# Optimization experiments

Measured on AMD Instinct MI355X. Metric: run time of the kernel, lower is better.

## Reference

```python
import jax, jax.numpy as jnp
import numpy as np

N_NODES = 50000
N_EDGES = 800000
F_IN = 128
HIDDEN = 128
F_OUT = 64
BN_EPS = 1e-5


def setup_inputs() -> dict:
    key = jax.random.key(0)
    ks = jax.random.split(key, 8)
    features = jax.random.normal(ks[0], (N_NODES, F_IN), dtype=jnp.float32)
    W1 = jax.random.normal(ks[1], (2 * F_IN, HIDDEN), dtype=jnp.float32) * 0.05
    b1 = jnp.zeros((HIDDEN,), dtype=jnp.float32)
    gamma = jnp.ones((HIDDEN,), dtype=jnp.float32)
    beta = jnp.zeros((HIDDEN,), dtype=jnp.float32)
    W2 = jax.random.normal(ks[2], (2 * HIDDEN, F_OUT), dtype=jnp.float32) * 0.05
    b2 = jnp.zeros((F_OUT,), dtype=jnp.float32)
    edge_vals = jax.random.uniform(ks[3], (N_EDGES,), dtype=jnp.float32)
    edge_src = jax.random.randint(ks[4], (N_EDGES,), 0, N_NODES, dtype=jnp.int32)
    edge_dst = jax.random.randint(ks[5], (N_EDGES,), 0, N_NODES, dtype=jnp.int32)
    return {"features": features, "W1": W1, "b1": b1, "gamma": gamma,
            "beta": beta, "W2": W2, "b2": b2, "edge_vals": edge_vals,
            "edge_src": edge_src, "edge_dst": edge_dst}


def _spmm(edge_vals, edge_src, edge_dst, x):
    # agg[i] = sum_{e: dst_e == i} w_e * x[src_e]   (sparse adjacency @ x)
    msgs = edge_vals[:, None] * x[edge_src]          # [E, d]
    return jax.ops.segment_sum(msgs, edge_dst, num_segments=N_NODES)


def _batchnorm(x, gamma, beta):
    # BatchNorm1d in training mode: batch stats, biased variance
    mean = jnp.mean(x, axis=0)
    var = jnp.mean(jnp.square(x - mean), axis=0)
    return gamma * (x - mean) * jax.lax.rsqrt(var + BN_EPS) + beta


def reference(features, W1, b1, gamma, beta, W2, b2, edge_vals, edge_src, edge_dst):
    # Layer 1: SpMM -> concat -> linear -> batchnorm -> relu  (dropout is a no-op, p=0)
    agg = _spmm(edge_vals, edge_src, edge_dst, features)     # [N, F_IN]
    s = jnp.concatenate([agg, features], axis=1)             # [N, 2*F_IN]
    h = s @ W1 + b1                                          # [N, HIDDEN]
    h = jax.nn.relu(_batchnorm(h, gamma, beta))
    # Layer 2: SpMM -> concat -> linear (identity act, no norm)
    agg2 = _spmm(edge_vals, edge_src, edge_dst, h)           # [N, HIDDEN]
    s2 = jnp.concatenate([agg2, h], axis=1)                  # [N, 2*HIDDEN]
    out = s2 @ W2 + b2                                       # [N, F_OUT]
    return out
```

## Files before the change

kernel.cpp:

```cpp
#include <hip/hip_runtime.h>

#define N_NODES 50000
#define N_EDGES 800000
#define F_IN    128
#define HID     128
#define F_OUT   64
#define BN_EPS  1e-5f

#define NRANGES 196
#define NCHUNKS 196
#define CHUNK   4096
#define CVT_BLOCKS 3125
#define PREPW_BLOCKS 24

typedef __bf16 bf16x8 __attribute__((ext_vector_type(8)));
typedef float  f32x4  __attribute__((ext_vector_type(4)));

static inline size_t align_up(size_t x, size_t a){ return (x + a - 1) / a * a; }

__device__ __forceinline__ float bflo(unsigned u){ return __uint_as_float(u << 16); }
__device__ __forceinline__ float bfhi(unsigned u){ return __uint_as_float(u & 0xffff0000u); }
__device__ __forceinline__ unsigned packbf(float a, float b){
  __bf16 ha = (__bf16)a, hb = (__bf16)b;
  unsigned short ua = __builtin_bit_cast(unsigned short, ha);
  unsigned short ub = __builtin_bit_cast(unsigned short, hb);
  return (unsigned)ua | ((unsigned)ub << 16);
}


__global__ __launch_bounds__(256) void k_setup(
    const int* __restrict__ dst, const float* __restrict__ X,
    const float* __restrict__ W1, const float* __restrict__ W2,
    int* __restrict__ Hcr, __bf16* __restrict__ Sx,
    __bf16* __restrict__ W1f, __bf16* __restrict__ W2f, float* __restrict__ bn_acc){
  __shared__ int hist[NRANGES];
  int b = blockIdx.x, t = threadIdx.x;
  if(b < NCHUNKS){
    if(t < NRANGES) hist[t] = 0;
    __syncthreads();
    int e0 = b * CHUNK;
    #pragma unroll
    for(int k = 0; k < CHUNK / 256; k++){
      int e = e0 + k * 256 + t;
      if(e < N_EDGES) atomicAdd(&hist[dst[e] >> 8], 1);
    }
    __syncthreads();
    if(t < NRANGES) Hcr[b * NRANGES + t] = hist[t];
  } else if(b < NCHUNKS + CVT_BLOCKS){
    int bb = b - NCHUNKS;
    if(bb == 0) bn_acc[t] = 0.f;
    int idx = bb * 256 + t;
    int n = idx >> 4;
    int c = (idx & 15) * 8;
    const float* xp = X + (size_t)n * F_IN + c;
    f32x4 x0 = *(const f32x4*)xp;
    f32x4 x1 = *(const f32x4*)(xp + 4);
    bf16x8 v;
    #pragma unroll
    for(int i = 0; i < 4; i++){ v[i] = (__bf16)x0[i]; v[4 + i] = (__bf16)x1[i]; }
    *(bf16x8*)(Sx + (size_t)n * 128 + c) = v;
  } else {
    int s = (b - NCHUNKS - CVT_BLOCKS) * 256 + t;
    if(s < 4096){
      int ks = s >> 9, rem = s & 511, nf = rem >> 6, l = rem & 63;
      int k = ks * 32 + (l >> 4) * 8, c = nf * 16 + (l & 15);
      bf16x8 v;
      #pragma unroll
      for(int i = 0; i < 8; i++) v[i] = (__bf16)W1[(size_t)(k + i) * HID + c];
      *(bf16x8*)(W1f + ((size_t)s << 3)) = v;
    } else {
      int q = s - 4096;
      int ks = q >> 9, rem = q & 511, nf = rem >> 6, l = rem & 63;
      int k = ks * 32 + (l >> 4) * 8, c = nf * 16 + (l & 15);
      bf16x8 v;
      #pragma unroll
      for(int i = 0; i < 8; i++){
        int kk = k + i;
        float val = (c < 64) ? W2[(size_t)kk * F_OUT + c]
                             : W2[(size_t)(HID + kk) * F_OUT + (c - 64)];
        v[i] = (__bf16)val;
      }
      *(bf16x8*)(W2f + ((size_t)q << 3)) = v;
    }
  }
}


__global__ __launch_bounds__(256) void k_scanR(int* __restrict__ Hcr, int* __restrict__ rtot){
  __shared__ int s[256];
  int r = blockIdx.x, t = threadIdx.x;
  int v = (t < NCHUNKS) ? Hcr[t * NRANGES + r] : 0;
  s[t] = v;
  __syncthreads();
  for(int off = 1; off < 256; off <<= 1){
    int u = (t >= off) ? s[t - off] : 0;
    __syncthreads();
    s[t] += u;
    __syncthreads();
  }
  if(t < NCHUNKS) Hcr[t * NRANGES + r] = s[t] - v;
  if(t == NCHUNKS - 1) rtot[r] = s[t];
}


__global__ __launch_bounds__(256) void k_pass2(const int* __restrict__ dst, const int* __restrict__ src,
    const float* __restrict__ vals, const int* __restrict__ Hcr,
    const int* __restrict__ rtot, int2* __restrict__ staged){
  __shared__ int s[256];
  __shared__ int cur[NRANGES];
  int c = blockIdx.x, t = threadIdx.x;
  int tv = (t < NRANGES) ? rtot[t] : 0;
  s[t] = tv;
  __syncthreads();
  for(int off = 1; off < 256; off <<= 1){
    int u = (t >= off) ? s[t - off] : 0;
    __syncthreads();
    s[t] += u;
    __syncthreads();
  }
  if(t < NRANGES) cur[t] = (s[t] - tv) + Hcr[c * NRANGES + t];
  __syncthreads();
  int e0 = c * CHUNK;
  #pragma unroll
  for(int k = 0; k < CHUNK / 256; k++){
    int e = e0 + k * 256 + t;
    if(e < N_EDGES){
      int d = dst[e];
      int pos = atomicAdd(&cur[d >> 8], 1);
      staged[pos] = make_int2(__float_as_int(vals[e]), src[e] | ((d & 255) << 16));
    }
  }
}


__global__ __launch_bounds__(256) void k_pass3(const int2* __restrict__ staged,
    const int* __restrict__ rtot, int2* __restrict__ epack, int* __restrict__ rp){
  __shared__ int s[256];
  __shared__ int cnt[256];
  __shared__ int begS, endS;
  int r = blockIdx.x, t = threadIdx.x;
  int tv = (t < NRANGES) ? rtot[t] : 0;
  s[t] = tv;
  __syncthreads();
  for(int off = 1; off < 256; off <<= 1){
    int u = (t >= off) ? s[t - off] : 0;
    __syncthreads();
    s[t] += u;
    __syncthreads();
  }
  if(t == r){ begS = s[t] - tv; endS = s[t]; }
  cnt[t] = 0;
  __syncthreads();
  int beg = begS, end = endS;
  for(int i = beg + t; i < end; i += 256)
    atomicAdd(&cnt[(staged[i].y >> 16) & 255], 1);
  __syncthreads();
  int v = cnt[t];
  s[t] = v;
  __syncthreads();
  for(int off = 1; off < 256; off <<= 1){
    int u = (t >= off) ? s[t - off] : 0;
    __syncthreads();
    s[t] += u;
    __syncthreads();
  }
  int excl = s[t] - v;
  int d = r * 256 + t;
  if(d < N_NODES) rp[d] = beg + excl;
  if(r == NRANGES - 1 && t == 0) rp[N_NODES] = N_EDGES;
  __syncthreads();
  cnt[t] = beg + excl;
  __syncthreads();
  for(int i = beg + t; i < end; i += 256){
    int2 e = staged[i];
    int dl = (e.y >> 16) & 255;
    int p = atomicAdd(&cnt[dl], 1);
    epack[p] = make_int2(e.x, e.y & 0xffff);
  }
}


__global__ __launch_bounds__(256) void k_spmm1(const __bf16* __restrict__ Sx,
    __bf16* __restrict__ Sa, const int2* __restrict__ epack, const int* __restrict__ rp){
  int w    = (int)((blockIdx.x * blockDim.x + threadIdx.x) >> 6);
  int lane = threadIdx.x & 63;
  if(w >= N_NODES) return;
  int beg = rp[w], end = rp[w + 1];
  float a0 = 0.f, a1 = 0.f;
  int e = beg;
  for(; e + 3 < end; e += 4){
    int2 p0 = epack[e], p1 = epack[e + 1], p2 = epack[e + 2], p3 = epack[e + 3];
    unsigned u0 = *(const unsigned*)(Sx + (size_t)p0.y * 128 + lane * 2);
    unsigned u1 = *(const unsigned*)(Sx + (size_t)p1.y * 128 + lane * 2);
    unsigned u2 = *(const unsigned*)(Sx + (size_t)p2.y * 128 + lane * 2);
    unsigned u3 = *(const unsigned*)(Sx + (size_t)p3.y * 128 + lane * 2);
    float w0 = __int_as_float(p0.x), w1 = __int_as_float(p1.x);
    float w2 = __int_as_float(p2.x), w3 = __int_as_float(p3.x);
    a0 = fmaf(w0, bflo(u0), a0); a1 = fmaf(w0, bfhi(u0), a1);
    a0 = fmaf(w1, bflo(u1), a0); a1 = fmaf(w1, bfhi(u1), a1);
    a0 = fmaf(w2, bflo(u2), a0); a1 = fmaf(w2, bfhi(u2), a1);
    a0 = fmaf(w3, bflo(u3), a0); a1 = fmaf(w3, bfhi(u3), a1);
  }
  for(; e < end; e++){
    int2 p = epack[e];
    float wt = __int_as_float(p.x);
    unsigned u = *(const unsigned*)(Sx + (size_t)p.y * 128 + lane * 2);
    a0 = fmaf(wt, bflo(u), a0); a1 = fmaf(wt, bfhi(u), a1);
  }
  *(unsigned*)(Sa + (size_t)w * 128 + lane * 2) = packbf(a0, a1);
}


__global__ __launch_bounds__(256) void k_gemm1(
    const __bf16* __restrict__ Sa, const __bf16* __restrict__ Sx,
    const __bf16* __restrict__ W1f, const float* __restrict__ b1,
    __bf16* __restrict__ hpre, float* __restrict__ bn_acc){
  __shared__ float bnred[2][256];
  const int tid = threadIdx.x;
  const int lane = tid & 63, wid = tid >> 6;
  const int wm = wid >> 1, wn = wid & 1;
  const int lr = lane & 15, lk = (lane >> 4) * 8;
  const int rbase = blockIdx.x * 64 + wm * 32 + lr;

  f32x4 acc[2][4];
  #pragma unroll
  for(int m = 0; m < 2; m++)
    #pragma unroll
    for(int n = 0; n < 4; n++) acc[m][n] = (f32x4){0.f, 0.f, 0.f, 0.f};

  for(int ks = 0; ks < 8; ks++){
    const __bf16* src = (ks < 4) ? Sa : Sx;
    const int kb = (ks & 3) * 32 + lk;
    bf16x8 a[2], b[4];
    #pragma unroll
    for(int m = 0; m < 2; m++){
      int r = rbase + m * 16; if(r > N_NODES - 1) r = N_NODES - 1;
      a[m] = *(const bf16x8*)(src + (size_t)r * 128 + kb);
    }
    #pragma unroll
    for(int n = 0; n < 4; n++)
      b[n] = *(const bf16x8*)(W1f + (((ks * 8 + wn * 4 + n) * 64 + lane) << 3));
    #pragma unroll
    for(int m = 0; m < 2; m++)
      #pragma unroll
      for(int n = 0; n < 4; n++)
        acc[m][n] = __builtin_amdgcn_mfma_f32_16x16x32_bf16(a[m], b[n], acc[m][n], 0, 0, 0);
  }

  #pragma unroll
  for(int n = 0; n < 4; n++){
    int gc = wn * 64 + n * 16 + lr;
    float bias = b1[gc];
    float ps = 0.f, pq = 0.f;
    #pragma unroll
    for(int m = 0; m < 2; m++){
      int gr0 = blockIdx.x * 64 + wm * 32 + m * 16 + (lane >> 4) * 4;
      #pragma unroll
      for(int i = 0; i < 4; i++){
        int r = gr0 + i;
        if(r < N_NODES){
          float h = acc[m][n][i] + bias;
          hpre[(size_t)r * HID + gc] = (__bf16)h;
          ps += h; pq += h * h;
        }
      }
    }
    ps += __shfl_xor(ps, 16); ps += __shfl_xor(ps, 32);
    pq += __shfl_xor(pq, 16); pq += __shfl_xor(pq, 32);
    if(lane < 16){
      bnred[wm][gc] = ps;
      bnred[wm][128 + gc] = pq;
    }
  }
  __syncthreads();
  atomicAdd(&bn_acc[tid], bnred[0][tid] + bnred[1][tid]);
}


__global__ __launch_bounds__(256) void k_gemm2(
    const __bf16* __restrict__ hpre, const __bf16* __restrict__ W2f,
    const float* __restrict__ b2, const float* __restrict__ bn_acc,
    const float* __restrict__ gamma, const float* __restrict__ beta,
    __bf16* __restrict__ y2b, float* __restrict__ out){
  __shared__ float s_scale[HID], s_shift[HID];
  const int tid = threadIdx.x;
  if(tid < HID){
    float mean = bn_acc[tid] / (float)N_NODES;
    float var  = bn_acc[HID + tid] / (float)N_NODES - mean * mean;
    float rs   = rsqrtf(var + BN_EPS);
    float sc   = gamma[tid] * rs;
    s_scale[tid] = sc;
    s_shift[tid] = beta[tid] - mean * sc;
  }
  const int lane = tid & 63, wid = tid >> 6;
  const int wm = wid >> 1, wn = wid & 1;
  const int lr = lane & 15, lk = (lane >> 4) * 8;
  const int rbase = blockIdx.x * 64 + wm * 32 + lr;

  f32x4 acc[2][4];
  #pragma unroll
  for(int m = 0; m < 2; m++)
    #pragma unroll
    for(int n = 0; n < 4; n++) acc[m][n] = (f32x4){0.f, 0.f, 0.f, 0.f};
  __syncthreads();

  for(int ks = 0; ks < 4; ks++){
    int k0 = ks * 32 + lk;
    f32x4 sc0 = *(const f32x4*)(s_scale + k0);
    f32x4 sc1 = *(const f32x4*)(s_scale + k0 + 4);
    f32x4 sh0 = *(const f32x4*)(s_shift + k0);
    f32x4 sh1 = *(const f32x4*)(s_shift + k0 + 4);
    bf16x8 a[2], b[4];
    #pragma unroll
    for(int m = 0; m < 2; m++){
      int r = rbase + m * 16; if(r > N_NODES - 1) r = N_NODES - 1;
      bf16x8 hv = *(const bf16x8*)(hpre + (size_t)r * HID + k0);
      bf16x8 af;
      #pragma unroll
      for(int i = 0; i < 4; i++){
        af[i]     = (__bf16)fmaxf(0.f, fmaf((float)hv[i],     sc0[i], sh0[i]));
        af[4 + i] = (__bf16)fmaxf(0.f, fmaf((float)hv[4 + i], sc1[i], sh1[i]));
      }
      a[m] = af;
    }
    #pragma unroll
    for(int n = 0; n < 4; n++)
      b[n] = *(const bf16x8*)(W2f + (((ks * 8 + wn * 4 + n) * 64 + lane) << 3));
    #pragma unroll
    for(int m = 0; m < 2; m++)
      #pragma unroll
      for(int n = 0; n < 4; n++)
        acc[m][n] = __builtin_amdgcn_mfma_f32_16x16x32_bf16(a[m], b[n], acc[m][n], 0, 0, 0);
  }

  #pragma unroll
  for(int n = 0; n < 4; n++){
    int c = n * 16 + lr;
    float bias = (wn == 1) ? b2[c] : 0.f;
    #pragma unroll
    for(int m = 0; m < 2; m++){
      int gr0 = blockIdx.x * 64 + wm * 32 + m * 16 + (lane >> 4) * 4;
      #pragma unroll
      for(int i = 0; i < 4; i++){
        int r = gr0 + i;
        if(r < N_NODES){
          if(wn == 0) y2b[(size_t)r * F_OUT + c] = (__bf16)acc[m][n][i];
          else        out[(size_t)r * F_OUT + c] = acc[m][n][i] + bias;
        }
      }
    }
  }
}


__global__ __launch_bounds__(256) void k_spmm2(const __bf16* __restrict__ y2b,
    const int2* __restrict__ epack, const int* __restrict__ rp, float* __restrict__ out){
  int w    = (int)((blockIdx.x * blockDim.x + threadIdx.x) >> 6);
  int lane = threadIdx.x & 63;
  if(w >= N_NODES) return;
  int beg = rp[w], end = rp[w + 1];
  int half = lane >> 5, li = lane & 31;
  float a0 = 0.f, a1 = 0.f;
  int e = beg + half;
  for(; e + 2 < end; e += 4){
    int2 p0 = epack[e], p1 = epack[e + 2];
    float w0 = __int_as_float(p0.x), w1 = __int_as_float(p1.x);
    unsigned u0 = *(const unsigned*)(y2b + (size_t)p0.y * F_OUT + li * 2);
    unsigned u1 = *(const unsigned*)(y2b + (size_t)p1.y * F_OUT + li * 2);
    a0 = fmaf(w0, bflo(u0), a0); a1 = fmaf(w0, bfhi(u0), a1);
    a0 = fmaf(w1, bflo(u1), a0); a1 = fmaf(w1, bfhi(u1), a1);
  }
  if(e < end){
    int2 p = epack[e];
    float wt = __int_as_float(p.x);
    unsigned u = *(const unsigned*)(y2b + (size_t)p.y * F_OUT + li * 2);
    a0 = fmaf(wt, bflo(u), a0); a1 = fmaf(wt, bfhi(u), a1);
  }
  a0 += __shfl_xor(a0, 32);
  a1 += __shfl_xor(a1, 32);
  if(lane < 32){
    float2 o = *(float2*)(out + (size_t)w * F_OUT + li * 2);
    o.x += a0; o.y += a1;
    *(float2*)(out + (size_t)w * F_OUT + li * 2) = o;
  }
}


extern "C" void kernel_launch(void* const* d_in, const int* in_sizes, int n_in,
                              void* d_out, int out_size, void* d_ws, size_t ws_size,
                              hipStream_t stream){
  const float* X     = (const float*)d_in[0];
  const float* W1    = (const float*)d_in[1];
  const float* b1    = (const float*)d_in[2];
  const float* gamma = (const float*)d_in[3];
  const float* beta  = (const float*)d_in[4];
  const float* W2    = (const float*)d_in[5];
  const float* b2    = (const float*)d_in[6];
  const float* evals = (const float*)d_in[7];
  const int*   esrc  = (const int*)d_in[8];
  const int*   edst  = (const int*)d_in[9];
  float* out = (float*)d_out;

  char* ws = (char*)d_ws;
  size_t off = 0;
  auto carve = [&](size_t bytes) -> char* {
    off = align_up(off, 256);
    char* p = ws + off;
    off += bytes;
    return p;
  };
  int*     Hcr    = (int*)    carve((size_t)NCHUNKS * NRANGES * 4);
  int*     rtot   = (int*)    carve((size_t)NRANGES * 4);
  int*     rp     = (int*)    carve(((size_t)N_NODES + 1) * 4);
  float*   bn_acc = (float*)  carve(256 * 4);
  int2*    staged = (int2*)   carve((size_t)N_EDGES * 8);
  int2*    epack  = (int2*)   carve((size_t)N_EDGES * 8);
  __bf16*  W1f    = (__bf16*) carve((size_t)4096 * 8 * 2);
  __bf16*  W2f    = (__bf16*) carve((size_t)2048 * 8 * 2);
  __bf16*  Sa     = (__bf16*) carve((size_t)N_NODES * 128 * 2);
  __bf16*  Sx     = (__bf16*) carve((size_t)N_NODES * 128 * 2);
  __bf16*  hpre   = (__bf16*) carve((size_t)N_NODES * HID * 2);
  __bf16*  y2b    = (__bf16*) carve((size_t)N_NODES * F_OUT * 2);

  k_setup<<<NCHUNKS + CVT_BLOCKS + PREPW_BLOCKS, 256, 0, stream>>>(
      edst, X, W1, W2, Hcr, Sx, W1f, W2f, bn_acc);
  k_scanR<<<NRANGES, 256, 0, stream>>>(Hcr, rtot);
  k_pass2<<<NCHUNKS, 256, 0, stream>>>(edst, esrc, evals, Hcr, rtot, staged);
  k_pass3<<<NRANGES, 256, 0, stream>>>(staged, rtot, epack, rp);

  k_spmm1<<<N_NODES / 4, 256, 0, stream>>>(Sx, Sa, epack, rp);
  k_gemm1<<<(N_NODES + 63) / 64, 256, 0, stream>>>(Sa, Sx, W1f, b1, hpre, bn_acc);
  k_gemm2<<<(N_NODES + 63) / 64, 256, 0, stream>>>(hpre, W2f, b2, bn_acc, gamma, beta, y2b, out);
  k_spmm2<<<N_NODES / 4, 256, 0, stream>>>(y2b, epack, rp, out);
}
```

Baseline: 245.7 us.

## Fuse CSR build kernels with grid barrier and pack edges as bf16 weight+index

Merges the three CSR-construction kernels (range scan, staging pass, per-range sort) into one persistent kernel of 196 blocks separated by atomic spin grid barriers, which removes two kernel launches and their gaps. Edge records shrink from 8-byte int2 to one 32-bit word holding a bf16 weight in the high half and a 16-bit source index in the low half, halving edge-list traffic in both SpMM kernels. The SpMM loops are unrolled further to keep more gathers in flight. The cost is lower precision on edge weights and a 16-bit index limit: N_NODES is 50000, so the index fits. The grid barrier relies on all 196 blocks being resident at the same time, which is assumed rather than guaranteed.

```diff
diff --git a/kernel.cpp b/kernel.cpp
--- a/kernel.cpp
+++ b/kernel.cpp
@@ -32,7 +32,8 @@
     const int* __restrict__ dst, const float* __restrict__ X,
     const float* __restrict__ W1, const float* __restrict__ W2,
     int* __restrict__ Hcr, __bf16* __restrict__ Sx,
-    __bf16* __restrict__ W1f, __bf16* __restrict__ W2f, float* __restrict__ bn_acc){
+    __bf16* __restrict__ W1f, __bf16* __restrict__ W2f,
+    float* __restrict__ bn_acc, int* __restrict__ bar){
   __shared__ int hist[NRANGES];
   int b = blockIdx.x, t = threadIdx.x;
   if(b < NCHUNKS){
@@ -48,7 +49,10 @@
     if(t < NRANGES) Hcr[b * NRANGES + t] = hist[t];
   } else if(b < NCHUNKS + CVT_BLOCKS){
     int bb = b - NCHUNKS;
-    if(bb == 0) bn_acc[t] = 0.f;
+    if(bb == 0){
+      bn_acc[t] = 0.f;
+      if(t < 2) bar[t] = 0;
+    }
     int idx = bb * 256 + t;
     int n = idx >> 4;
     int c = (idx & 15) * 8;
@@ -86,125 +90,156 @@
 }
 
 
-__global__ __launch_bounds__(256) void k_scanR(int* __restrict__ Hcr, int* __restrict__ rtot){
+__device__ __forceinline__ void grid_bar(int* bar, int n){
+  __syncthreads();
+  if(threadIdx.x == 0){
+    __threadfence();
+    atomicAdd(bar, 1);
+    while(atomicAdd(bar, 0) < n){ }
+    __threadfence();
+  }
+  __syncthreads();
+}
+
+__global__ __launch_bounds__(256) void k_csr(
+    const int* __restrict__ dst, const int* __restrict__ src, const float* __restrict__ vals,
+    int* __restrict__ Hcr, int* __restrict__ rtot, int2* __restrict__ staged,
+    unsigned* __restrict__ epack, int* __restrict__ rp, int* __restrict__ bar){
   __shared__ int s[256];
-  int r = blockIdx.x, t = threadIdx.x;
-  int v = (t < NCHUNKS) ? Hcr[t * NRANGES + r] : 0;
-  s[t] = v;
-  __syncthreads();
-  for(int off = 1; off < 256; off <<= 1){
-    int u = (t >= off) ? s[t - off] : 0;
-    __syncthreads();
-    s[t] += u;
-    __syncthreads();
-  }
-  if(t < NCHUNKS) Hcr[t * NRANGES + r] = s[t] - v;
-  if(t == NCHUNKS - 1) rtot[r] = s[t];
-}
-
-
-__global__ __launch_bounds__(256) void k_pass2(const int* __restrict__ dst, const int* __restrict__ src,
-    const float* __restrict__ vals, const int* __restrict__ Hcr,
-    const int* __restrict__ rtot, int2* __restrict__ staged){
-  __shared__ int s[256];
-  __shared__ int cur[NRANGES];
-  int c = blockIdx.x, t = threadIdx.x;
-  int tv = (t < NRANGES) ? rtot[t] : 0;
-  s[t] = tv;
-  __syncthreads();
-  for(int off = 1; off < 256; off <<= 1){
-    int u = (t >= off) ? s[t - off] : 0;
-    __syncthreads();
-    s[t] += u;
-    __syncthreads();
-  }
-  if(t < NRANGES) cur[t] = (s[t] - tv) + Hcr[c * NRANGES + t];
-  __syncthreads();
-  int e0 = c * CHUNK;
-  #pragma unroll
-  for(int k = 0; k < CHUNK / 256; k++){
-    int e = e0 + k * 256 + t;
-    if(e < N_EDGES){
-      int d = dst[e];
-      int pos = atomicAdd(&cur[d >> 8], 1);
-      staged[pos] = make_int2(__float_as_int(vals[e]), src[e] | ((d & 255) << 16));
-    }
-  }
-}
-
-
-__global__ __launch_bounds__(256) void k_pass3(const int2* __restrict__ staged,
-    const int* __restrict__ rtot, int2* __restrict__ epack, int* __restrict__ rp){
-  __shared__ int s[256];
-  __shared__ int cnt[256];
+  __shared__ int aux[256];
   __shared__ int begS, endS;
-  int r = blockIdx.x, t = threadIdx.x;
-  int tv = (t < NRANGES) ? rtot[t] : 0;
-  s[t] = tv;
-  __syncthreads();
-  for(int off = 1; off < 256; off <<= 1){
-    int u = (t >= off) ? s[t - off] : 0;
-    __syncthreads();
-    s[t] += u;
-    __syncthreads();
-  }
-  if(t == r){ begS = s[t] - tv; endS = s[t]; }
-  cnt[t] = 0;
-  __syncthreads();
-  int beg = begS, end = endS;
-  for(int i = beg + t; i < end; i += 256)
-    atomicAdd(&cnt[(staged[i].y >> 16) & 255], 1);
-  __syncthreads();
-  int v = cnt[t];
-  s[t] = v;
-  __syncthreads();
-  for(int off = 1; off < 256; off <<= 1){
-    int u = (t >= off) ? s[t - off] : 0;
-    __syncthreads();
-    s[t] += u;
-    __syncthreads();
-  }
-  int excl = s[t] - v;
-  int d = r * 256 + t;
-  if(d < N_NODES) rp[d] = beg + excl;
-  if(r == NRANGES - 1 && t == 0) rp[N_NODES] = N_EDGES;
-  __syncthreads();
-  cnt[t] = beg + excl;
-  __syncthreads();
-  for(int i = beg + t; i < end; i += 256){
-    int2 e = staged[i];
-    int dl = (e.y >> 16) & 255;
-    int p = atomicAdd(&cnt[dl], 1);
-    epack[p] = make_int2(e.x, e.y & 0xffff);
+  const int b = blockIdx.x, t = threadIdx.x;
+
+  {
+    int v = (t < NCHUNKS) ? Hcr[t * NRANGES + b] : 0;
+    s[t] = v;
+    __syncthreads();
+    for(int off = 1; off < 256; off <<= 1){
+      int u = (t >= off) ? s[t - off] : 0;
+      __syncthreads();
+      s[t] += u;
+      __syncthreads();
+    }
+    if(t < NCHUNKS) Hcr[t * NRANGES + b] = s[t] - v;
+    if(t == NCHUNKS - 1) rtot[b] = s[t];
+  }
+  grid_bar(&bar[0], NRANGES);
+
+  {
+    int tv = (t < NRANGES) ? rtot[t] : 0;
+    s[t] = tv;
+    __syncthreads();
+    for(int off = 1; off < 256; off <<= 1){
+      int u = (t >= off) ? s[t - off] : 0;
+      __syncthreads();
+      s[t] += u;
+      __syncthreads();
+    }
+    if(t < NRANGES) aux[t] = (s[t] - tv) + Hcr[b * NRANGES + t];
+    __syncthreads();
+    int e0 = b * CHUNK;
+    #pragma unroll
+    for(int k = 0; k < CHUNK / 256; k++){
+      int e = e0 + k * 256 + t;
+      if(e < N_EDGES){
+        int d = dst[e];
+        int pos = atomicAdd(&aux[d >> 8], 1);
+        staged[pos] = make_int2(__float_as_int(vals[e]), src[e] | ((d & 255) << 16));
+      }
+    }
+  }
+  grid_bar(&bar[1], NRANGES);
+
+  {
+    int tv = (t < NRANGES) ? rtot[t] : 0;
+    s[t] = tv;
+    __syncthreads();
+    for(int off = 1; off < 256; off <<= 1){
+      int u = (t >= off) ? s[t - off] : 0;
+      __syncthreads();
+      s[t] += u;
+      __syncthreads();
+    }
+    if(t == b){ begS = s[t] - tv; endS = s[t]; }
+    aux[t] = 0;
+    __syncthreads();
+    int beg = begS, end = endS;
+    for(int i = beg + t; i < end; i += 256)
+      atomicAdd(&aux[(staged[i].y >> 16) & 255], 1);
+    __syncthreads();
+    int v = aux[t];
+    s[t] = v;
+    __syncthreads();
+    for(int off = 1; off < 256; off <<= 1){
+      int u = (t >= off) ? s[t - off] : 0;
+      __syncthreads();
+      s[t] += u;
+      __syncthreads();
+    }
+    int excl = s[t] - v;
+    int d = b * 256 + t;
+    if(d < N_NODES) rp[d] = beg + excl;
+    if(b == NRANGES - 1 && t == 0) rp[N_NODES] = N_EDGES;
+    __syncthreads();
+    aux[t] = beg + excl;
+    __syncthreads();
+    for(int i = beg + t; i < end; i += 256){
+      int2 e = staged[i];
+      int dl = (e.y >> 16) & 255;
+      int p = atomicAdd(&aux[dl], 1);
+      unsigned wb = (unsigned)__builtin_bit_cast(unsigned short, (__bf16)__int_as_float(e.x));
+      epack[p] = (wb << 16) | (unsigned)(e.y & 0xffff);
+    }
   }
 }
 
 
 __global__ __launch_bounds__(256) void k_spmm1(const __bf16* __restrict__ Sx,
-    __bf16* __restrict__ Sa, const int2* __restrict__ epack, const int* __restrict__ rp){
+    __bf16* __restrict__ Sa, const unsigned* __restrict__ epack, const int* __restrict__ rp){
   int w    = (int)((blockIdx.x * blockDim.x + threadIdx.x) >> 6);
   int lane = threadIdx.x & 63;
   if(w >= N_NODES) return;
   int beg = rp[w], end = rp[w + 1];
   float a0 = 0.f, a1 = 0.f;
   int e = beg;
-  for(; e + 3 < end; e += 4){
-    int2 p0 = epack[e], p1 = epack[e + 1], p2 = epack[e + 2], p3 = epack[e + 3];
-    unsigned u0 = *(const unsigned*)(Sx + (size_t)p0.y * 128 + lane * 2);
-    unsigned u1 = *(const unsigned*)(Sx + (size_t)p1.y * 128 + lane * 2);
-    unsigned u2 = *(const unsigned*)(Sx + (size_t)p2.y * 128 + lane * 2);
-    unsigned u3 = *(const unsigned*)(Sx + (size_t)p3.y * 128 + lane * 2);
-    float w0 = __int_as_float(p0.x), w1 = __int_as_float(p1.x);
-    float w2 = __int_as_float(p2.x), w3 = __int_as_float(p3.x);
+  for(; e + 7 < end; e += 8){
+    unsigned q0 = epack[e],     q1 = epack[e + 1], q2 = epack[e + 2], q3 = epack[e + 3];
+    unsigned q4 = epack[e + 4], q5 = epack[e + 5], q6 = epack[e + 6], q7 = epack[e + 7];
+    unsigned u0 = *(const unsigned*)(Sx + (size_t)(q0 & 0xffff) * 128 + lane * 2);
+    unsigned u1 = *(const unsigned*)(Sx + (size_t)(q1 & 0xffff) * 128 + lane * 2);
+    unsigned u2 = *(const unsigned*)(Sx + (size_t)(q2 & 0xffff) * 128 + lane * 2);
+    unsigned u3 = *(const unsigned*)(Sx + (size_t)(q3 & 0xffff) * 128 + lane * 2);
+    unsigned u4 = *(const unsigned*)(Sx + (size_t)(q4 & 0xffff) * 128 + lane * 2);
+    unsigned u5 = *(const unsigned*)(Sx + (size_t)(q5 & 0xffff) * 128 + lane * 2);
+    unsigned u6 = *(const unsigned*)(Sx + (size_t)(q6 & 0xffff) * 128 + lane * 2);
+    unsigned u7 = *(const unsigned*)(Sx + (size_t)(q7 & 0xffff) * 128 + lane * 2);
+    float w0 = bfhi(q0), w1 = bfhi(q1), w2 = bfhi(q2), w3 = bfhi(q3);
+    float w4 = bfhi(q4), w5 = bfhi(q5), w6 = bfhi(q6), w7 = bfhi(q7);
     a0 = fmaf(w0, bflo(u0), a0); a1 = fmaf(w0, bfhi(u0), a1);
     a0 = fmaf(w1, bflo(u1), a0); a1 = fmaf(w1, bfhi(u1), a1);
     a0 = fmaf(w2, bflo(u2), a0); a1 = fmaf(w2, bfhi(u2), a1);
     a0 = fmaf(w3, bflo(u3), a0); a1 = fmaf(w3, bfhi(u3), a1);
+    a0 = fmaf(w4, bflo(u4), a0); a1 = fmaf(w4, bfhi(u4), a1);
+    a0 = fmaf(w5, bflo(u5), a0); a1 = fmaf(w5, bfhi(u5), a1);
+    a0 = fmaf(w6, bflo(u6), a0); a1 = fmaf(w6, bfhi(u6), a1);
+    a0 = fmaf(w7, bflo(u7), a0); a1 = fmaf(w7, bfhi(u7), a1);
+  }
+  for(; e + 3 < end; e += 4){
+    unsigned q0 = epack[e], q1 = epack[e + 1], q2 = epack[e + 2], q3 = epack[e + 3];
+    unsigned u0 = *(const unsigned*)(Sx + (size_t)(q0 & 0xffff) * 128 + lane * 2);
+    unsigned u1 = *(const unsigned*)(Sx + (size_t)(q1 & 0xffff) * 128 + lane * 2);
+    unsigned u2 = *(const unsigned*)(Sx + (size_t)(q2 & 0xffff) * 128 + lane * 2);
+    unsigned u3 = *(const unsigned*)(Sx + (size_t)(q3 & 0xffff) * 128 + lane * 2);
+    float w0 = bfhi(q0), w1 = bfhi(q1), w2 = bfhi(q2), w3 = bfhi(q3);
+    a0 = fmaf(w0, bflo(u0), a0); a1 = fmaf(w0, bfhi(u0), a1);
+    a0 = fmaf(w1, bflo(u1), a0); a1 = fmaf(w1, bfhi(u1), a1);
+    a0 = fmaf(w2, bflo(u2), a0); a1 = fmaf(w2, bfhi(u2), a1);
+    a0 = fmaf(w3, bflo(u3), a0); a1 = fmaf(w3, bfhi(u3), a1);
   }
   for(; e < end; e++){
-    int2 p = epack[e];
-    float wt = __int_as_float(p.x);
-    unsigned u = *(const unsigned*)(Sx + (size_t)p.y * 128 + lane * 2);
+    unsigned q = epack[e];
+    float wt = bfhi(q);
+    unsigned u = *(const unsigned*)(Sx + (size_t)(q & 0xffff) * 128 + lane * 2);
     a0 = fmaf(wt, bflo(u), a0); a1 = fmaf(wt, bfhi(u), a1);
   }
   *(unsigned*)(Sa + (size_t)w * 128 + lane * 2) = packbf(a0, a1);
@@ -354,7 +389,7 @@
 
 
 __global__ __launch_bounds__(256) void k_spmm2(const __bf16* __restrict__ y2b,
-    const int2* __restrict__ epack, const int* __restrict__ rp, float* __restrict__ out){
+    const unsigned* __restrict__ epack, const int* __restrict__ rp, float* __restrict__ out){
   int w    = (int)((blockIdx.x * blockDim.x + threadIdx.x) >> 6);
   int lane = threadIdx.x & 63;
   if(w >= N_NODES) return;
@@ -362,18 +397,23 @@
   int half = lane >> 5, li = lane & 31;
   float a0 = 0.f, a1 = 0.f;
   int e = beg + half;
-  for(; e + 2 < end; e += 4){
-    int2 p0 = epack[e], p1 = epack[e + 2];
-    float w0 = __int_as_float(p0.x), w1 = __int_as_float(p1.x);
-    unsigned u0 = *(const unsigned*)(y2b + (size_t)p0.y * F_OUT + li * 2);
-    unsigned u1 = *(const unsigned*)(y2b + (size_t)p1.y * F_OUT + li * 2);
+  for(; e + 6 < end; e += 8){
+    unsigned q0 = epack[e],     q1 = epack[e + 2];
+    unsigned q2 = epack[e + 4], q3 = epack[e + 6];
+    unsigned u0 = *(const unsigned*)(y2b + (size_t)(q0 & 0xffff) * F_OUT + li * 2);
+    unsigned u1 = *(const unsigned*)(y2b + (size_t)(q1 & 0xffff) * F_OUT + li * 2);
+    unsigned u2 = *(const unsigned*)(y2b + (size_t)(q2 & 0xffff) * F_OUT + li * 2);
+    unsigned u3 = *(const unsigned*)(y2b + (size_t)(q3 & 0xffff) * F_OUT + li * 2);
+    float w0 = bfhi(q0), w1 = bfhi(q1), w2 = bfhi(q2), w3 = bfhi(q3);
     a0 = fmaf(w0, bflo(u0), a0); a1 = fmaf(w0, bfhi(u0), a1);
     a0 = fmaf(w1, bflo(u1), a0); a1 = fmaf(w1, bfhi(u1), a1);
-  }
-  if(e < end){
-    int2 p = epack[e];
-    float wt = __int_as_float(p.x);
-    unsigned u = *(const unsigned*)(y2b + (size_t)p.y * F_OUT + li * 2);
+    a0 = fmaf(w2, bflo(u2), a0); a1 = fmaf(w2, bfhi(u2), a1);
+    a0 = fmaf(w3, bflo(u3), a0); a1 = fmaf(w3, bfhi(u3), a1);
+  }
+  for(; e < end; e += 2){
+    unsigned q = epack[e];
+    float wt = bfhi(q);
+    unsigned u = *(const unsigned*)(y2b + (size_t)(q & 0xffff) * F_OUT + li * 2);
     a0 = fmaf(wt, bflo(u), a0); a1 = fmaf(wt, bfhi(u), a1);
   }
   a0 += __shfl_xor(a0, 32);
@@ -409,24 +449,23 @@
     off += bytes;
     return p;
   };
-  int*     Hcr    = (int*)    carve((size_t)NCHUNKS * NRANGES * 4);
-  int*     rtot   = (int*)    carve((size_t)NRANGES * 4);
-  int*     rp     = (int*)    carve(((size_t)N_NODES + 1) * 4);
-  float*   bn_acc = (float*)  carve(256 * 4);
-  int2*    staged = (int2*)   carve((size_t)N_EDGES * 8);
-  int2*    epack  = (int2*)   carve((size_t)N_EDGES * 8);
-  __bf16*  W1f    = (__bf16*) carve((size_t)4096 * 8 * 2);
-  __bf16*  W2f    = (__bf16*) carve((size_t)2048 * 8 * 2);
-  __bf16*  Sa     = (__bf16*) carve((size_t)N_NODES * 128 * 2);
-  __bf16*  Sx     = (__bf16*) carve((size_t)N_NODES * 128 * 2);
-  __bf16*  hpre   = (__bf16*) carve((size_t)N_NODES * HID * 2);
-  __bf16*  y2b    = (__bf16*) carve((size_t)N_NODES * F_OUT * 2);
+  int*      Hcr    = (int*)     carve((size_t)NCHUNKS * NRANGES * 4);
+  int*      rtot   = (int*)     carve((size_t)NRANGES * 4);
+  int*      rp     = (int*)     carve(((size_t)N_NODES + 1) * 4);
+  float*    bn_acc = (float*)   carve(256 * 4);
+  int*      bar    = (int*)     carve(64 * 4);
+  int2*     staged = (int2*)    carve((size_t)N_EDGES * 8);
+  unsigned* epack  = (unsigned*)carve((size_t)N_EDGES * 4);
+  __bf16*   W1f    = (__bf16*)  carve((size_t)4096 * 8 * 2);
+  __bf16*   W2f    = (__bf16*)  carve((size_t)2048 * 8 * 2);
+  __bf16*   Sa     = (__bf16*)  carve((size_t)N_NODES * 128 * 2);
+  __bf16*   Sx     = (__bf16*)  carve((size_t)N_NODES * 128 * 2);
+  __bf16*   hpre   = (__bf16*)  carve((size_t)N_NODES * HID * 2);
+  __bf16*   y2b    = (__bf16*)  carve((size_t)N_NODES * F_OUT * 2);
 
   k_setup<<<NCHUNKS + CVT_BLOCKS + PREPW_BLOCKS, 256, 0, stream>>>(
-      edst, X, W1, W2, Hcr, Sx, W1f, W2f, bn_acc);
-  k_scanR<<<NRANGES, 256, 0, stream>>>(Hcr, rtot);
-  k_pass2<<<NCHUNKS, 256, 0, stream>>>(edst, esrc, evals, Hcr, rtot, staged);
-  k_pass3<<<NRANGES, 256, 0, stream>>>(staged, rtot, epack, rp);
+      edst, X, W1, W2, Hcr, Sx, W1f, W2f, bn_acc, bar);
+  k_csr<<<NRANGES, 256, 0, stream>>>(edst, esrc, evals, Hcr, rtot, staged, epack, rp, bar);
 
   k_spmm1<<<N_NODES / 4, 256, 0, stream>>>(Sx, Sa, epack, rp);
   k_gemm1<<<(N_NODES + 63) / 64, 256, 0, stream>>>(Sa, Sx, W1f, b1, hpre, bn_acc);
```

New measurement: 259.4 us. 5.6% more time.
